# Kernel optimization log

Hardware: AMD Instinct MI355X
Metric: run time of the kernel (lower is better)

Reference implementation:

```python
import jax, jax.numpy as jnp
import numpy as np

B, TX, TY, C, H = 16, 256, 2048, 80, 256
NEG = -1e9


def setup_inputs() -> dict:
    key = jax.random.key(0)
    k = jax.random.split(key, 6)
    en = jax.random.normal(k[0], (B, H, TX), jnp.float32)           # encoder out [B,H,Tx]
    mu = jax.random.normal(k[1], (B, C, TX), jnp.float32)           # MDN means [B,C,Tx]
    log_sigma = 0.1 * jax.random.normal(k[2], (B, C, TX), jnp.float32)
    y = jax.random.normal(k[3], (B, TY, C), jnp.float32)            # mel target [B,Ty,C]
    # lengths near max so y_len >= x_len (monotonic path exists)
    x_lengths = TX - jax.random.randint(k[4], (B,), 0, 64, dtype=jnp.int32)
    y_lengths = TY - jax.random.randint(k[5], (B,), 0, 512, dtype=jnp.int32)
    return {"en": en, "mu": mu, "log_sigma": log_sigma, "y": y,
            "x_lengths": x_lengths, "y_lengths": y_lengths}


def compute_log_probs(mu, log_sigma, y):
    """logp[b,x,t] = -0.5*mean_c[(y[b,t,c]-mu[b,x,c])^2/sigma^2] - 0.5*mean_c[log_sigma].
    Expanded as y^2 - 2*y*mu + mu^2 to avoid materializing [B,Tx,Ty,C]."""
    mu_t = jnp.swapaxes(mu, 1, 2)          # [B,Tx,C]
    ls_t = jnp.swapaxes(log_sigma, 1, 2)   # [B,Tx,C]
    inv_var = jnp.exp(-2.0 * ls_t)         # 1/sigma^2
    t1 = jnp.einsum('byc,bxc->bxy', y * y, inv_var)
    t2 = jnp.einsum('byc,bxc->bxy', y, mu_t * inv_var)
    t3 = jnp.sum(mu_t * mu_t * inv_var, axis=-1)[..., None]
    expo = -0.5 * (t1 - 2.0 * t2 + t3) / C
    return expo - 0.5 * jnp.mean(ls_t, axis=-1, keepdims=True)  # [B,Tx,Ty]


def _mas_single(logp, x_len, y_len):
    """Viterbi monotonic alignment search for one batch item. logp: [Tx,Ty]."""
    tx, ty = logp.shape
    ii = jnp.arange(tx)
    row_ok = ii < x_len

    def fwd(v_prev, col):
        shifted = jnp.concatenate([jnp.full((1,), NEG, v_prev.dtype), v_prev[:-1]])
        diag = shifted > v_prev                      # came from i-1
        v = jnp.maximum(v_prev, shifted) + col
        v = jnp.where(row_ok, v, NEG)
        return v, diag

    v0 = jnp.where(ii == 0, 0.0, NEG).astype(logp.dtype)
    _, diag = jax.lax.scan(fwd, v0, jnp.swapaxes(logp, 0, 1))  # diag: [Ty,Tx] bool

    def bwd(idx, inp):
        d_j, j = inp
        active = j < y_len
        row = jnp.where(active, (ii == idx).astype(logp.dtype), 0.0)
        new_idx = jnp.where(active, idx - d_j[idx].astype(idx.dtype), idx)
        new_idx = jnp.maximum(new_idx, 0)
        return new_idx, row

    idx0 = (x_len - 1).astype(jnp.int32)
    _, rows = jax.lax.scan(bwd, idx0, (diag, jnp.arange(ty)), reverse=True)
    return jnp.swapaxes(rows, 0, 1)  # path [Tx,Ty]


def maximum_path(logp, x_lengths, y_lengths):
    return jax.vmap(_mas_single)(logp, x_lengths, y_lengths)


def generate_path(dr, x_mask, y_mask):
    """Durations [B,Tx] -> hard alignment [B,Tx,Ty]."""
    cum = jnp.cumsum(dr, axis=-1)                                  # [B,Tx]
    j = jnp.arange(y_mask.shape[-1], dtype=dr.dtype)
    m = (j[None, None, :] < cum[:, :, None]).astype(dr.dtype)      # [B,Tx,Ty]
    path = m - jnp.concatenate([jnp.zeros_like(m[:, :1]), m[:, :-1]], axis=1)
    return path * (x_mask[:, :, None] * y_mask[:, None, :])


def reference(en, mu, log_sigma, y, x_lengths, y_lengths):
    x_mask = (jnp.arange(TX)[None, :] < x_lengths[:, None]).astype(en.dtype)
    y_mask = (jnp.arange(TY)[None, :] < y_lengths[:, None]).astype(en.dtype)
    logp = compute_log_probs(mu, log_sigma, y)                     # [B,Tx,Ty]
    attn_mas = jax.lax.stop_gradient(maximum_path(logp, x_lengths, y_lengths))
    dr_mas = jnp.sum(attn_mas, axis=-1)                            # [B,Tx]
    attn = generate_path(dr_mas, x_mask, y_mask)                   # [B,Tx,Ty]
    o_en_ex = jnp.einsum('bxy,bcx->bcy', attn, en)                 # [B,H,Ty]
    return (o_en_ex, attn, dr_mas, logp)
```

## Files before the change

kernel.cpp:

```cpp
#include <hip/hip_runtime.h>
#include <hip/hip_bf16.h>
#include <cstdint>
#include <cstddef>

#define B_ 16
#define TX_ 256
#define TY_ 2048
#define C_ 80
#define H_ 256
#define NEG_ -1e9f
#define NEG_I (int)0xCE6E6B28

#define BT_STEP(JB)                                                           \
    {                                                                         \
        unsigned bit = ((unsigned)(W >> (((ii & 7) << 3)                      \
                                         | (7 - (JB)))) & 1u)                 \
                     & (unsigned)(ii > 0);                                    \
        ii -= (int)bit;                                                       \
        W = (bit && ((ii & 7) == 7)) ? Wl : W;                                \
    }

__global__ __launch_bounds__(256) void logp_kernel(
    const float* __restrict__ mu, const float* __restrict__ ls,
    const float* __restrict__ y, float* __restrict__ logp_out,
    float* __restrict__ logp_t)
{
    __shared__ float2 coef[16 * 80];
    __shared__ float  aux[16 * 80];
    __shared__ float  Kx[16];
    __shared__ float  yt[16 * 1028];

    const int tid = threadIdx.x;
    const int t0 = blockIdx.x * 1024;
    const int x0 = blockIdx.y * 16;
    const int b  = blockIdx.z;

    for (int i = tid; i < 16 * 80; i += 256) {
        int c = i >> 4, x = i & 15;
        float m = mu[(size_t)(b * C_ + c) * TX_ + x0 + x];
        float l = ls[(size_t)(b * C_ + c) * TX_ + x0 + x];
        float w = __expf(-2.f * l);
        coef[x * 80 + c] = make_float2(w, -2.f * m * w);
        aux[x * 80 + c]  = fmaf(m * m, w, l);
    }
    __syncthreads();
    if (tid < 16) {
        float s = 0.f;
        for (int c = 0; c < C_; ++c) s += aux[tid * 80 + c];
        Kx[tid] = -0.5f * s / (float)C_;
    }

    float acc[16][4];
#pragma unroll
    for (int x = 0; x < 16; ++x)
#pragma unroll
        for (int r = 0; r < 4; ++r) acc[x][r] = 0.f;

    const float4* y4 = (const float4*)y;
    for (int c0 = 0; c0 < C_; c0 += 16) {
        __syncthreads();
        for (int it = 0; it < 16; ++it) {
            int f = tid + it * 256;
            int t = f >> 2, k = f & 3;
            float4 v = y4[(size_t)(b * TY_ + t0 + t) * 20 + (c0 >> 2) + k];
            yt[(4 * k + 0) * 1028 + t] = v.x;
            yt[(4 * k + 1) * 1028 + t] = v.y;
            yt[(4 * k + 2) * 1028 + t] = v.z;
            yt[(4 * k + 3) * 1028 + t] = v.w;
        }
        __syncthreads();
        for (int cl = 0; cl < 16; ++cl) {
            const float4 yv = *reinterpret_cast<const float4*>(&yt[cl * 1028 + 4 * tid]);
            float4 y2 = make_float4(yv.x * yv.x, yv.y * yv.y, yv.z * yv.z, yv.w * yv.w);
#pragma unroll
            for (int x = 0; x < 16; ++x) {
                float2 f2 = coef[x * 80 + c0 + cl];
                acc[x][0] = fmaf(y2.x, f2.x, fmaf(yv.x, f2.y, acc[x][0]));
                acc[x][1] = fmaf(y2.y, f2.x, fmaf(yv.y, f2.y, acc[x][1]));
                acc[x][2] = fmaf(y2.z, f2.x, fmaf(yv.z, f2.y, acc[x][2]));
                acc[x][3] = fmaf(y2.w, f2.x, fmaf(yv.w, f2.y, acc[x][3]));
            }
        }
    }

#pragma unroll
    for (int x = 0; x < 16; ++x) {
        float kx = Kx[x];
#pragma unroll
        for (int r = 0; r < 4; ++r) acc[x][r] = fmaf(acc[x][r], -0.5f / (float)C_, kx);
        float4 out = make_float4(acc[x][0], acc[x][1], acc[x][2], acc[x][3]);
        *reinterpret_cast<float4*>(
            &logp_out[(size_t)(b * TX_ + x0 + x) * TY_ + t0 + 4 * tid]) = out;
    }
#pragma unroll
    for (int r = 0; r < 4; ++r) {
#pragma unroll
        for (int q = 0; q < 4; ++q) {
            float4 out = make_float4(acc[4 * q + 0][r], acc[4 * q + 1][r],
                                     acc[4 * q + 2][r], acc[4 * q + 3][r]);
            *reinterpret_cast<float4*>(
                &logp_t[(size_t)(b * TY_ + t0 + 4 * tid + r) * TX_ + x0 + 4 * q]) = out;
        }
    }
}

#define PROQ(A, Bq, Cq, Dq) \
    "global_load_dwordx4 " A ", %[vo], %[sb]\n\t" \
    "global_load_dwordx4 " Bq ", %[vo], %[sb] offset:0x400\n\t" \
    "global_load_dwordx4 " Cq ", %[vo], %[sb] offset:0x800\n\t" \
    "global_load_dwordx4 " Dq ", %[vo], %[sb] offset:0xC00\n\t" \
    "v_add_u32 %[vo], 0x1000, %[vo]\n\t"

#define ADDVO "v_add_u32 %[vo], 0x1000, %[vo]\n\t"

#define COLN(RQ, R0, R1, R2, R3, SHU, SHD, OFF) \
    "v_cmp_gt_f32 vcc, " SHU ", %[v0]\n\t" \
    "v_cmp_gt_f32 s[20:21], %[v0], %[v1]\n\t" \
    "v_cmp_gt_f32 s[22:23], %[v1], %[v2]\n\t" \
    "v_cmp_gt_f32 s[24:25], %[v2], %[v3]\n\t" \
    "v_max_f32 %[v3], %[v2], %[v3]\n\t" \
    "v_max_f32 %[v2], %[v1], %[v2]\n\t" \
    "v_add_f32 %[v3], " R3 ", %[v3]\n\t" \
    "v_max_f32 %[v1], %[v0], %[v1]\n\t" \
    "v_max_f32 %[v0], " SHU ", %[v0]\n\t" \
    "v_mov_b32_dpp " SHD ", %[v3] wave_shr:1 row_mask:0xf bank_mask:0xf\n\t" \
    "v_add_f32 %[v2], " R2 ", %[v2]\n\t" \
    "v_add_f32 %[v1], " R1 ", %[v1]\n\t" \
    "v_add_f32 %[v0], " R0 ", %[v0]\n\t" \
    "v_addc_co_u32 %[a0], vcc, %[a0], %[a0], vcc\n\t" \
    "v_addc_co_u32 %[a1], s[20:21], %[a1], %[a1], s[20:21]\n\t" \
    "v_addc_co_u32 %[a2], s[22:23], %[a2], %[a2], s[22:23]\n\t" \
    "v_addc_co_u32 %[a3], s[24:25], %[a3], %[a3], s[24:25]\n\t" \
    "global_load_dwordx4 " RQ ", %[vo], %[sb] offset:" OFF "\n\t"

#define STOREBLK(OFFD) \
    "v_lshl_or_b32 v29, %[a1], 8, %[a0]\n\t" \
    "v_lshl_or_b32 v29, %[a2], 16, v29\n\t" \
    "v_lshl_or_b32 v29, %[a3], 24, v29\n\t" \
    "global_store_dword %[df], v29, %[db] offset:" OFFD "\n\t" \
    "v_mov_b32 %[a0], 0\n\t" \
    "v_mov_b32 %[a1], 0\n\t" \
    "v_mov_b32 %[a2], 0\n\t" \
    "v_mov_b32 %[a3], 0\n\t"

#define WAITG "s_waitcnt vmcnt(24)\n\t"

__global__ __launch_bounds__(64, 1) void mas_fwd_kernel(
    const float* __restrict__ logp_t, unsigned int* __restrict__ diag_g)
{
    const int lane = threadIdx.x;
    const int b = blockIdx.x;

    uint64_t sb = (uint64_t)(logp_t + (size_t)b * TY_ * TX_);
    uint64_t db = (uint64_t)(diag_g + (size_t)b * (TY_ / 8) * 64);
    unsigned vo = (unsigned)(lane * 16);
    unsigned df = (unsigned)(lane * 4);

    float v0 = (lane == 0) ? 0.f : NEG_, v1 = NEG_, v2 = NEG_, v3 = NEG_;
    unsigned a0 = 0, a1 = 0, a2 = 0, a3 = 0;

    asm volatile(
        "v_mov_b32 v28, 0xce6e6b28\n\t"
        "v_mov_b32 v30, 0xce6e6b28\n\t"
        PROQ("v[32:35]",   "v[36:39]",   "v[40:43]",   "v[44:47]")
        PROQ("v[48:51]",   "v[52:55]",   "v[56:59]",   "v[60:63]")
        PROQ("v[64:67]",   "v[68:71]",   "v[72:75]",   "v[76:79]")
        PROQ("v[80:83]",   "v[84:87]",   "v[88:91]",   "v[92:95]")
        PROQ("v[96:99]",   "v[100:103]", "v[104:107]", "v[108:111]")
        PROQ("v[112:115]", "v[116:119]", "v[120:123]", "v[124:127]")
        PROQ("v[128:131]", "v[132:135]", "v[136:139]", "v[140:143]")
        PROQ("v[144:147]", "v[148:151]", "v[152:155]", "v[156:159]")
        "s_mov_b32 s26, 64\n\t"
        "Lmas_%=:\n\t"
        WAITG
        COLN("v[32:35]", "v32", "v33", "v34", "v35", "v28", "v30", "0")
        COLN("v[36:39]", "v36", "v37", "v38", "v39", "v30", "v28", "0x400")
        COLN("v[40:43]", "v40", "v41", "v42", "v43", "v28", "v30", "0x800")
        COLN("v[44:47]", "v44", "v45", "v46", "v47", "v30", "v28", "0xC00")
        ADDVO
        COLN("v[48:51]", "v48", "v49", "v50", "v51", "v28", "v30", "0")
        COLN("v[52:55]", "v52", "v53", "v54", "v55", "v30", "v28", "0x400")
        COLN("v[56:59]", "v56", "v57", "v58", "v59", "v28", "v30", "0x800")
        COLN("v[60:63]", "v60", "v61", "v62", "v63", "v30", "v28", "0xC00")
        ADDVO
        STOREBLK("0")
        WAITG
        COLN("v[64:67]", "v64", "v65", "v66", "v67", "v28", "v30", "0")
        COLN("v[68:71]", "v68", "v69", "v70", "v71", "v30", "v28", "0x400")
        COLN("v[72:75]", "v72", "v73", "v74", "v75", "v28", "v30", "0x800")
        COLN("v[76:79]", "v76", "v77", "v78", "v79", "v30", "v28", "0xC00")
        ADDVO
        COLN("v[80:83]", "v80", "v81", "v82", "v83", "v28", "v30", "0")
        COLN("v[84:87]", "v84", "v85", "v86", "v87", "v30", "v28", "0x400")
        COLN("v[88:91]", "v88", "v89", "v90", "v91", "v28", "v30", "0x800")
        COLN("v[92:95]", "v92", "v93", "v94", "v95", "v30", "v28", "0xC00")
        ADDVO
        STOREBLK("0x100")
        WAITG
        COLN("v[96:99]",   "v96",  "v97",  "v98",  "v99",  "v28", "v30", "0")
        COLN("v[100:103]", "v100", "v101", "v102", "v103", "v30", "v28", "0x400")
        COLN("v[104:107]", "v104", "v105", "v106", "v107", "v28", "v30", "0x800")
        COLN("v[108:111]", "v108", "v109", "v110", "v111", "v30", "v28", "0xC00")
        ADDVO
        COLN("v[112:115]", "v112", "v113", "v114", "v115", "v28", "v30", "0")
        COLN("v[116:119]", "v116", "v117", "v118", "v119", "v30", "v28", "0x400")
        COLN("v[120:123]", "v120", "v121", "v122", "v123", "v28", "v30", "0x800")
        COLN("v[124:127]", "v124", "v125", "v126", "v127", "v30", "v28", "0xC00")
        ADDVO
        STOREBLK("0x200")
        WAITG
        COLN("v[128:131]", "v128", "v129", "v130", "v131", "v28", "v30", "0")
        COLN("v[132:135]", "v132", "v133", "v134", "v135", "v30", "v28", "0x400")
        COLN("v[136:139]", "v136", "v137", "v138", "v139", "v28", "v30", "0x800")
        COLN("v[140:143]", "v140", "v141", "v142", "v143", "v30", "v28", "0xC00")
        ADDVO
        COLN("v[144:147]", "v144", "v145", "v146", "v147", "v28", "v30", "0")
        COLN("v[148:151]", "v148", "v149", "v150", "v151", "v30", "v28", "0x400")
        COLN("v[152:155]", "v152", "v153", "v154", "v155", "v28", "v30", "0x800")
        COLN("v[156:159]", "v156", "v157", "v158", "v159", "v30", "v28", "0xC00")
        ADDVO
        STOREBLK("0x300")
        "v_add_u32 %[df], 0x400, %[df]\n\t"
        "s_sub_u32 s26, s26, 1\n\t"
        "s_cmp_lg_u32 s26, 0\n\t"
        "s_cbranch_scc1 Lmas_%=\n\t"
        : [v0]"+v"(v0), [v1]"+v"(v1), [v2]"+v"(v2), [v3]"+v"(v3),
          [a0]"+v"(a0), [a1]"+v"(a1), [a2]"+v"(a2), [a3]"+v"(a3),
          [vo]"+v"(vo), [df]"+v"(df)
        : [sb]"s"(sb), [db]"s"(db)
        : "vcc", "scc", "memory",
          "s20","s21","s22","s23","s24","s25","s26",
          "v28","v29","v30",
          "v32","v33","v34","v35","v36","v37","v38","v39",
          "v40","v41","v42","v43","v44","v45","v46","v47",
          "v48","v49","v50","v51","v52","v53","v54","v55",
          "v56","v57","v58","v59","v60","v61","v62","v63",
          "v64","v65","v66","v67","v68","v69","v70","v71",
          "v72","v73","v74","v75","v76","v77","v78","v79",
          "v80","v81","v82","v83","v84","v85","v86","v87",
          "v88","v89","v90","v91","v92","v93","v94","v95",
          "v96","v97","v98","v99","v100","v101","v102","v103",
          "v104","v105","v106","v107","v108","v109","v110","v111",
          "v112","v113","v114","v115","v116","v117","v118","v119",
          "v120","v121","v122","v123","v124","v125","v126","v127",
          "v128","v129","v130","v131","v132","v133","v134","v135",
          "v136","v137","v138","v139","v140","v141","v142","v143",
          "v144","v145","v146","v147","v148","v149","v150","v151",
          "v152","v153","v154","v155","v156","v157","v158","v159");
}

__global__ __launch_bounds__(256) void mas_tab_kernel(
    const unsigned int* __restrict__ diag_g, unsigned char* __restrict__ E_g,
    unsigned char* __restrict__ E2_g)
{
    __shared__ unsigned char El[16][256];
    const int t  = threadIdx.x;
    const int cg = blockIdx.x;
    const int b  = blockIdx.y;
    const unsigned int* dg = diag_g + (size_t)b * (TY_ / 8) * 64;
    unsigned char* Eb = E_g + (size_t)b * (TY_ / 8) * 256;
    const int p = t >> 3;

    for (int k = 0; k < 16; ++k) {
        const int c = cg * 16 + k;
        unsigned long long W  = *(const unsigned long long*)&dg[c * 64 + 2 * p];
        unsigned long long Wl = p > 0
            ? *(const unsigned long long*)&dg[c * 64 + 2 * (p - 1)] : 0ULL;
        int ii = t;
#pragma unroll
        for (int jb = 7; jb >= 0; --jb) BT_STEP(jb)
        Eb[c * 256 + t] = (unsigned char)ii;
        El[k][t] = (unsigned char)ii;
    }
    __syncthreads();
    int ii = t;
#pragma unroll
    for (int k = 15; k >= 0; --k) ii = El[k][ii];
    E2_g[((size_t)b * 16 + cg) * 256 + t] = (unsigned char)ii;
}

__global__ __launch_bounds__(256) void mas_bt_kernel(
    const unsigned int* __restrict__ diag_g, const unsigned char* __restrict__ E_g,
    const unsigned char* __restrict__ E2_g,
    const int* __restrict__ xlen, const int* __restrict__ ylen,
    float* __restrict__ dr_out, int* __restrict__ idx_out)
{
    __shared__ unsigned char E[256 * 256];
    __shared__ unsigned char E2l[16 * 256];
    __shared__ unsigned char entry_s[256];
    __shared__ unsigned char cg_entry[16];
    __shared__ int rows_l[TY_];
    __shared__ int cnt_l[TX_];
    const int tid = threadIdx.x;
    const int b = blockIdx.x;
    const int x_len = xlen[b];
    const int y_len = ylen[b];

    cnt_l[tid] = 0;

    const uint4* srcE = (const uint4*)(E_g + (size_t)b * (TY_ / 8) * 256);
    uint4* dstE = (uint4*)E;
#pragma unroll
    for (int it = 0; it < 16; ++it)
        dstE[tid + it * 256] = srcE[tid + it * 256];
    const uint4* srcE2 = (const uint4*)(E2_g + (size_t)b * 16 * 256);
    ((uint4*)E2l)[tid] = srcE2[tid];
    __syncthreads();

    const unsigned int* dg = diag_g + (size_t)b * (TY_ / 8) * 64;
    int* ib = idx_out + (size_t)b * TY_;
    const int jc = (y_len - 1) >> 3;
    const int cg0 = jc >> 4;

    if (tid == 0) {
        int ii = x_len - 1;
        int p = ii >> 3;
        unsigned long long W  = *(const unsigned long long*)&dg[jc * 64 + 2 * p];
        unsigned long long Wl = p > 0
            ? *(const unsigned long long*)&dg[jc * 64 + 2 * (p - 1)] : 0ULL;
        for (int jb = (y_len - 1) & 7; jb >= 0; --jb) {
            int j = 8 * jc + jb;
            ib[j] = ii; rows_l[j] = ii;
            BT_STEP(jb)
        }
        int cur = ii;
        for (int c = jc - 1; c >= cg0 * 16; --c) {
            entry_s[c] = (unsigned char)cur;
            cur = E[c * 256 + cur];
        }
        for (int cg = cg0 - 1; cg >= 0; --cg) {
            cg_entry[cg] = (unsigned char)cur;
            cur = E2l[cg * 256 + cur];
        }
    }
    __syncthreads();

    if (tid < cg0) {
        int cur = cg_entry[tid];
        for (int k = 15; k >= 0; --k) {
            int c = tid * 16 + k;
            entry_s[c] = (unsigned char)cur;
            cur = E[c * 256 + cur];
        }
    }
    __syncthreads();

    if (tid < jc) {
        const int c = tid;
        int ii = entry_s[c];
        int p = ii >> 3;
        unsigned long long W  = *(const unsigned long long*)&dg[c * 64 + 2 * p];
        unsigned long long Wl = p > 0
            ? *(const unsigned long long*)&dg[c * 64 + 2 * (p - 1)] : 0ULL;
        int r[8];
#pragma unroll
        for (int jb = 7; jb >= 0; --jb) {
            r[jb] = ii;
            BT_STEP(jb)
        }
        *reinterpret_cast<int4*>(&ib[8 * c])     = make_int4(r[0], r[1], r[2], r[3]);
        *reinterpret_cast<int4*>(&ib[8 * c + 4]) = make_int4(r[4], r[5], r[6], r[7]);
        *reinterpret_cast<int4*>(&rows_l[8 * c])     = make_int4(r[0], r[1], r[2], r[3]);
        *reinterpret_cast<int4*>(&rows_l[8 * c + 4]) = make_int4(r[4], r[5], r[6], r[7]);
    }
    __syncthreads();

    for (int t = tid; t < TY_; t += 256)
        if (t < y_len) atomicAdd(&cnt_l[rows_l[t]], 1);
    __syncthreads();
    dr_out[(size_t)b * TX_ + tid] = (float)cnt_l[tid];
}

__global__ __launch_bounds__(256) void emit_kernel(
    const float* __restrict__ en, const int* __restrict__ ylen,
    const int* __restrict__ idx_in, float* __restrict__ o_en,
    float* __restrict__ attn)
{
    const int tid = threadIdx.x;
    const int b = blockIdx.x;
    const int r = blockIdx.y;
    const int y_len = ylen[b];
    const int* ib = idx_in + (size_t)b * TY_;

    if (r < 256) {
        const int x = r;
        float* out = attn + ((size_t)b * TX_ + x) * TY_;
        for (int t = tid; t < TY_; t += 256) {
            int ii = ib[t];
            out[t] = (t < y_len && ii == x) ? 1.f : 0.f;
        }
    } else {
        const int h = r - 256;
        __shared__ float enr[256];
        enr[tid] = en[((size_t)b * H_ + h) * TX_ + tid];
        __syncthreads();
        float* out = o_en + ((size_t)b * H_ + h) * TY_;
        for (int t = tid; t < TY_; t += 256) {
            int ii = ib[t];
            bool a = (t < y_len);
            int is = a ? ii : 0;
            out[t] = a ? enr[is] : 0.f;
        }
    }
}

__global__ __launch_bounds__(256) void emit_sparse_kernel(
    const float* __restrict__ en, const int* __restrict__ ylen,
    const int* __restrict__ idx_in, float* __restrict__ o_en,
    float* __restrict__ attn)
{
    const int tid = threadIdx.x;
    const int b = blockIdx.x;
    const int r = blockIdx.y;
    const int y_len = ylen[b];
    const int* ib = idx_in + (size_t)b * TY_;

    if (r == 256) {
        float* ab = attn + (size_t)b * TX_ * TY_;
        for (int t = tid; t < TY_; t += 256)
            if (t < y_len) ab[(size_t)ib[t] * TY_ + t] = 1.f;
    } else {
        const int h = r;
        __shared__ float enr[256];
        enr[tid] = en[((size_t)b * H_ + h) * TX_ + tid];
        __syncthreads();
        float* out = o_en + ((size_t)b * H_ + h) * TY_;
        for (int t = tid; t < TY_; t += 256) {
            int ii = ib[t];
            bool a = (t < y_len);
            int is = a ? ii : 0;
            out[t] = a ? enr[is] : 0.f;
        }
    }
}

extern "C" void kernel_launch(void* const* d_in, const int* in_sizes, int n_in,
                              void* d_out, int out_size, void* d_ws, size_t ws_size,
                              hipStream_t stream)
{
    const float* en = (const float*)d_in[0];
    const float* mu = (const float*)d_in[1];
    const float* ls = (const float*)d_in[2];
    const float* y  = (const float*)d_in[3];
    const int* xl   = (const int*)d_in[4];
    const int* yl   = (const int*)d_in[5];

    float* o_en = (float*)d_out;
    float* attn = o_en + (size_t)B_ * TX_ * TY_;
    float* dr   = attn + (size_t)B_ * TX_ * TY_;
    float* logp = dr + (size_t)B_ * TX_;

    const size_t logp_t_bytes = (size_t)B_ * TX_ * TY_ * 4;
    const size_t E_bytes      = (size_t)B_ * (TY_ / 8) * 256;
    const size_t idx_bytes    = (size_t)B_ * TY_ * 4;

    unsigned int* diag_g = (unsigned int*)o_en;
    unsigned char* E2_g = (unsigned char*)o_en + (1u << 21);

    float* logp_t;
    unsigned char* E_g;
    int* idxArr;
    bool sparse;
    if (ws_size >= logp_t_bytes + E_bytes + idx_bytes) {
        logp_t = (float*)d_ws;
        E_g    = (unsigned char*)d_ws + logp_t_bytes;
        idxArr = (int*)((char*)d_ws + logp_t_bytes + E_bytes);
        sparse = true;
    } else {
        logp_t = attn;
        E_g    = (unsigned char*)attn;
        idxArr = (int*)d_ws;
        sparse = false;
    }

    dim3 g1(2, 16, 16);
    logp_kernel<<<g1, 256, 0, stream>>>(mu, ls, y, logp, logp_t);

    mas_fwd_kernel<<<dim3(16), dim3(64), 0, stream>>>(logp_t, diag_g);
    mas_tab_kernel<<<dim3(16, 16), dim3(256), 0, stream>>>(diag_g, E_g, E2_g);
    mas_bt_kernel<<<dim3(16), dim3(256), 0, stream>>>(diag_g, E_g, E2_g,
                                                      xl, yl, dr, idxArr);

    if (sparse) {
        dim3 g3(16, 257);
        emit_sparse_kernel<<<g3, 256, 0, stream>>>(en, yl, idxArr, o_en, attn);
    } else {
        dim3 g3(16, 512);
        emit_kernel<<<g3, 256, 0, stream>>>(en, yl, idxArr, o_en, attn);
    }
}
```

Baseline: 276.6 us.

## Overlap logp output transpose with serial MAS forward pass

The logp kernel no longer writes the [B,Tx,Ty] logp output directly and writes only the transposed copy. The MAS forward kernel gets 256 extra blocks that rebuild the logp output from the transposed buffer through a shared-memory tile transpose. These blocks run alongside the 16 latency-bound single-wave Viterbi blocks, and those waves raise their scheduling priority with s_setprio. The intent is to hide the logp write traffic behind the serial DP, at the cost of an extra read of logp_t and possible memory contention with the DP's streaming loads.

```diff
diff --git a/kernel.cpp b/kernel.cpp
--- a/kernel.cpp
+++ b/kernel.cpp
@@ -22,8 +22,7 @@
 
 __global__ __launch_bounds__(256) void logp_kernel(
     const float* __restrict__ mu, const float* __restrict__ ls,
-    const float* __restrict__ y, float* __restrict__ logp_out,
-    float* __restrict__ logp_t)
+    const float* __restrict__ y, float* __restrict__ logp_t)
 {
     __shared__ float2 coef[16 * 80];
     __shared__ float  aux[16 * 80];
@@ -88,9 +87,6 @@
         float kx = Kx[x];
 #pragma unroll
         for (int r = 0; r < 4; ++r) acc[x][r] = fmaf(acc[x][r], -0.5f / (float)C_, kx);
-        float4 out = make_float4(acc[x][0], acc[x][1], acc[x][2], acc[x][3]);
-        *reinterpret_cast<float4*>(
-            &logp_out[(size_t)(b * TX_ + x0 + x) * TY_ + t0 + 4 * tid]) = out;
     }
 #pragma unroll
     for (int r = 0; r < 4; ++r) {
@@ -145,10 +141,34 @@
 
 #define WAITG "s_waitcnt vmcnt(24)\n\t"
 
-__global__ __launch_bounds__(64, 1) void mas_fwd_kernel(
-    const float* __restrict__ logp_t, unsigned int* __restrict__ diag_g)
-{
-    const int lane = threadIdx.x;
+__global__ __launch_bounds__(256, 1) void mas_fwd_kernel(
+    const float* __restrict__ logp_t, unsigned int* __restrict__ diag_g,
+    float* __restrict__ logp_out)
+{
+    __shared__ float tile[64][65];
+    const int tid = threadIdx.x;
+
+    if (blockIdx.x >= 16) {
+        const int cb = blockIdx.x - 16;
+        const int b  = cb >> 4;
+        const int s  = cb & 15;
+        const int wv = tid >> 6, ln = tid & 63;
+        for (int ti = 0; ti < 8; ++ti) {
+            int tile_id = s * 8 + ti;
+            int x0 = (tile_id & 3) * 64;
+            int t0 = (tile_id >> 2) * 64;
+            for (int r = wv; r < 64; r += 4)
+                tile[r][ln] = logp_t[((size_t)b * TY_ + t0 + r) * TX_ + x0 + ln];
+            __syncthreads();
+            for (int r = wv; r < 64; r += 4)
+                logp_out[((size_t)b * TX_ + x0 + r) * TY_ + t0 + ln] = tile[ln][r];
+            __syncthreads();
+        }
+        return;
+    }
+    if (tid >= 64) return;
+
+    const int lane = tid;
     const int b = blockIdx.x;
 
     uint64_t sb = (uint64_t)(logp_t + (size_t)b * TY_ * TX_);
@@ -160,6 +180,7 @@
     unsigned a0 = 0, a1 = 0, a2 = 0, a3 = 0;
 
     asm volatile(
+        "s_setprio 3\n\t"
         "v_mov_b32 v28, 0xce6e6b28\n\t"
         "v_mov_b32 v30, 0xce6e6b28\n\t"
         PROQ("v[32:35]",   "v[36:39]",   "v[40:43]",   "v[44:47]")
@@ -474,9 +495,9 @@
     }
 
     dim3 g1(2, 16, 16);
-    logp_kernel<<<g1, 256, 0, stream>>>(mu, ls, y, logp, logp_t);
-
-    mas_fwd_kernel<<<dim3(16), dim3(64), 0, stream>>>(logp_t, diag_g);
+    logp_kernel<<<g1, 256, 0, stream>>>(mu, ls, y, logp_t);
+
+    mas_fwd_kernel<<<dim3(16 + 256), dim3(256), 0, stream>>>(logp_t, diag_g, logp);
     mas_tab_kernel<<<dim3(16, 16), dim3(256), 0, stream>>>(diag_g, E_g, E2_g);
     mas_bt_kernel<<<dim3(16), dim3(256), 0, stream>>>(diag_g, E_g, E2_g,
                                                       xl, yl, dr, idxArr);
```

New measurement: 280.2 us. Within noise of the previous version (+1.3%).
